# Kernel optimization log

Hardware: AMD Instinct MI355X
Metric: run time of the kernel (lower is better)

## Reference

```python
import jax, jax.numpy as jnp
import numpy as np

G, NPG = 100, 500
N = G * NPG            # 50000 nodes, contiguous equal-size graphs
IN, H = 128, 256
L = 3                  # num_layers
K = 3                  # knn k (loop=True -> self included)
E = 16 * N             # 800000 edges

def setup_inputs():
    key = jax.random.key(0)
    k = jax.random.split(key, 8)
    x = jax.random.normal(k[0], (N, IN), jnp.float32)
    batch = jnp.repeat(jnp.arange(G, dtype=jnp.int32), NPG)
    gid = jax.random.randint(k[1], (E,), 0, G)
    src = jax.random.randint(k[2], (E,), 0, NPG) + gid * NPG
    dst = jax.random.randint(k[3], (E,), 0, NPG) + gid * NPG
    edge_index = jnp.stack([src, dst]).astype(jnp.int32)
    def lin(kk, fin, fout):
        return (jax.random.normal(kk, (fin, fout), jnp.float32) / np.sqrt(fin)).astype(jnp.float32)
    inp = dict(x=x, edge_index=edge_index, batch=batch)
    inp["emb_W"] = lin(k[4], IN, H); inp["emb_b"] = jnp.zeros((H,), jnp.float32)
    inp["conv_W"] = jnp.stack([lin(jax.random.fold_in(k[5], i), H, H) for i in range(L)])
    inp["conv_b"] = jnp.zeros((L, H), jnp.float32)
    inp["fconv_W"] = jnp.stack([lin(jax.random.fold_in(k[6], i), H, H) for i in range(L)])
    inp["fconv_b"] = jnp.zeros((L, H), jnp.float32)
    inp["norm_w"] = jnp.ones((L, H), jnp.float32); inp["norm_b"] = jnp.zeros((L, H), jnp.float32); inp["norm_ms"] = jnp.ones((L, H), jnp.float32)
    inp["fnorm_w"] = jnp.ones((L, H), jnp.float32); inp["fnorm_b"] = jnp.zeros((L, H), jnp.float32); inp["fnorm_ms"] = jnp.ones((L, H), jnp.float32)
    inp["gate_W"] = lin(k[7], 2 * H, H); inp["gate_b"] = jnp.zeros((H,), jnp.float32)
    return inp

def _gcn_conv(h, src, dst, W, b):
    # GCNConv: add self loops, symmetric deg^-1/2 normalization
    m = h @ W                                     # [N,H]
    loop = jnp.arange(N, dtype=src.dtype)
    s2 = jnp.concatenate([src, loop]); d2 = jnp.concatenate([dst, loop])
    deg = jax.ops.segment_sum(jnp.ones_like(d2, jnp.float32), d2, num_segments=N)
    dinv = jnp.where(deg > 0, jax.lax.rsqrt(deg), 0.0)
    coef = (dinv[s2] * dinv[d2])[:, None]
    return jax.ops.segment_sum(m[s2] * coef, d2, num_segments=N) + b

def _graph_norm(x, batch, w, b, ms, cnt):
    # PyG GraphNorm: out = w * (x - ms*mean) / sqrt(var + eps) + b, per-graph stats
    mean = jax.ops.segment_sum(x, batch, num_segments=G) / cnt
    out = x - mean[batch] * ms
    var = jax.ops.segment_sum(out * out, batch, num_segments=G) / cnt
    return w * out * jax.lax.rsqrt(var + 1e-5)[batch] + b

def _knn_graph(x):
    # per-graph cosine knn, loop=True (self has sim 1 and is kept)
    xr = x.reshape(G, NPG, -1)
    xn = xr / (jnp.linalg.norm(xr, axis=-1, keepdims=True) + 1e-12)
    sim = jnp.einsum('gnh,gmh->gnm', xn, xn)      # [G,NPG,NPG]
    _, idx = jax.lax.top_k(sim, K)                # [G,NPG,K]
    offs = (jnp.arange(G) * NPG)[:, None, None]
    src = (idx + offs).reshape(-1)
    dst = jnp.broadcast_to(jnp.arange(N).reshape(G, NPG, 1), (G, NPG, K)).reshape(-1)
    return src.astype(jnp.int32), dst.astype(jnp.int32)

def reference(x, edge_index, batch, emb_W, emb_b, conv_W, conv_b, norm_w, norm_b, norm_ms, fconv_W, fconv_b, fnorm_w, fnorm_b, fnorm_ms, gate_W, gate_b):
    cnt = jax.ops.segment_sum(jnp.ones((N,), jnp.float32), batch, num_segments=G)[:, None]
    h = x @ emb_W + emb_b
    fsrc, fdst = _knn_graph(h)
    src, dst = edge_index[0], edge_index[1]
    all_x = []
    for i in range(L - 1):   # eval mode: dropout is identity
        prev = h
        h = _gcn_conv(h, src, dst, conv_W[i], conv_b[i])
        h = jax.nn.leaky_relu(_graph_norm(h, batch, norm_w[i], norm_b[i], norm_ms[i], cnt))
        f = _gcn_conv(h, fsrc, fdst, fconv_W[i], fconv_b[i])
        f = jax.nn.leaky_relu(_graph_norm(f, batch, fnorm_w[i], fnorm_b[i], fnorm_ms[i], cnt))
        gate = jax.nn.sigmoid(jnp.concatenate([h, f], axis=-1) @ gate_W + gate_b)
        h = gate * h + (1.0 - gate) * f + prev
        all_x.append(h)
    # faithful to source: for i in range(L): += pool(all_x[i-1])  (Python negative indexing!)
    gf = jnp.zeros((G, H), jnp.float32)
    for i in range(L):
        gf = gf + jax.ops.segment_sum(all_x[i - 1], batch, num_segments=G) / cnt
    return gf
```

## Files before the change

kernel.cpp:

```cpp
#include <hip/hip_runtime.h>
#include <math.h>

#define NN 50000
#define GG 100
#define NPGc 500
#define HH 256
#define IND 128

typedef __attribute__((ext_vector_type(8))) short short8v;
typedef __attribute__((ext_vector_type(4))) float f32x4;

__device__ __forceinline__ ushort f2bf(float f) {
    union { float f; unsigned u; } v; v.f = f;
    unsigned r = (v.u + 0x7fffu + ((v.u >> 16) & 1u)) >> 16;
    return (ushort)r;
}
__device__ __forceinline__ float bf2f(ushort h) {
    union { unsigned u; float f; } v; v.u = ((unsigned)h) << 16;
    return v.f;
}

__device__ __forceinline__ int swz(int row, int kidx) { return kidx ^ ((row & 7) << 3); }

__global__ void wcvt(const float* __restrict__ src, ushort* __restrict__ dst, int K, int N)
{
    int i = blockIdx.x * 256 + threadIdx.x;
    if (i < K * N) {
        int n = i / K, k = i % K;
        dst[i] = f2bf(src[(size_t)k * N + n]);
    }
}

__global__ __launch_bounds__(256)
void gemm_mfma(const void* __restrict__ Av, const void* __restrict__ A2v, int abf,
               const ushort* __restrict__ Wt, const float* __restrict__ bias,
               float* __restrict__ C, ushort* __restrict__ Cbf,
               int M, int K, int lda, int mode,
               const ushort* __restrict__ hn, const ushort* __restrict__ fn,
               const void* __restrict__ prevv, int prevbf)
{
    __shared__ ushort As[128][64];
    __shared__ ushort Bs[128][64];
    const int tid = threadIdx.x;
    const int lane = tid & 63;
    const int w = tid >> 6;
    const int wr = (w >> 1) * 64, wc = (w & 1) * 64;
    const int row0 = blockIdx.x * 128, col0 = blockIdx.y * 128;
    const int lr = lane & 15, lk = (lane >> 4) * 8;
    f32x4 acc[4][4] = {};

    for (int k0 = 0; k0 < K; k0 += 64) {
        __syncthreads();
        #pragma unroll
        for (int it = 0; it < 4; ++it) {
            int c = it * 256 + tid;
            int row = c >> 3, col = (c & 7) * 8;
            int gr = row0 + row; if (gr > M - 1) gr = M - 1;
            int kk = k0 + col;
            if (abf) {
                const ushort* Ap = (const ushort*)Av;
                if (A2v != nullptr && kk >= 256) { Ap = (const ushort*)A2v; kk -= 256; }
                *(int4*)&As[row][swz(row, col)] =
                    *(const int4*)&Ap[(size_t)gr * lda + kk];
            } else {
                const float* Ap = (const float*)Av;
                if (A2v != nullptr && kk >= 256) { Ap = (const float*)A2v; kk -= 256; }
                const float* s = &Ap[(size_t)gr * lda + kk];
                float4 v0 = *(const float4*)s;
                float4 v1 = *(const float4*)(s + 4);
                union { ushort u[8]; int4 q; } pk;
                pk.u[0] = f2bf(v0.x); pk.u[1] = f2bf(v0.y); pk.u[2] = f2bf(v0.z); pk.u[3] = f2bf(v0.w);
                pk.u[4] = f2bf(v1.x); pk.u[5] = f2bf(v1.y); pk.u[6] = f2bf(v1.z); pk.u[7] = f2bf(v1.w);
                *(int4*)&As[row][swz(row, col)] = pk.q;
            }
        }
        #pragma unroll
        for (int it = 0; it < 4; ++it) {
            int c = it * 256 + tid;
            int n = c >> 3, k = (c & 7) * 8;
            *(int4*)&Bs[n][swz(n, k)] = *(const int4*)&Wt[(size_t)(col0 + n) * K + k0 + k];
        }
        __syncthreads();
        #pragma unroll
        for (int ks = 0; ks < 2; ++ks) {
            short8v av[4], bv[4];
            #pragma unroll
            for (int m = 0; m < 4; ++m) {
                int rr = wr + m * 16 + lr;
                av[m] = *(const short8v*)&As[rr][swz(rr, ks * 32 + lk)];
            }
            #pragma unroll
            for (int n = 0; n < 4; ++n) {
                int rr = wc + n * 16 + lr;
                bv[n] = *(const short8v*)&Bs[rr][swz(rr, ks * 32 + lk)];
            }
            #pragma unroll
            for (int m = 0; m < 4; ++m)
                #pragma unroll
                for (int n = 0; n < 4; ++n)
                    acc[m][n] = __builtin_amdgcn_mfma_f32_16x16x32_bf16(av[m], bv[n], acc[m][n], 0, 0, 0);
        }
    }
    const int fr = (lane >> 4) * 4;
    if (mode == 0) {
        #pragma unroll
        for (int n = 0; n < 4; ++n) {
            int col = col0 + wc + n * 16 + lr;
            float bb = bias ? bias[col] : 0.f;
            #pragma unroll
            for (int m = 0; m < 4; ++m) {
                int rbase = row0 + wr + m * 16 + fr;
                #pragma unroll
                for (int r = 0; r < 4; ++r) {
                    int row = rbase + r;
                    if (row < M) C[(size_t)row * HH + col] = acc[m][n][r] + bb;
                }
            }
        }
    } else if (mode == 2) {
        #pragma unroll
        for (int n = 0; n < 4; ++n) {
            int col = col0 + wc + n * 16 + lr;
            float bb = bias ? bias[col] : 0.f;
            #pragma unroll
            for (int m = 0; m < 4; ++m) {
                int rbase = row0 + wr + m * 16 + fr;
                #pragma unroll
                for (int r = 0; r < 4; ++r) {
                    int row = rbase + r;
                    if (row < M) Cbf[(size_t)row * HH + col] = f2bf(acc[m][n][r] + bb);
                }
            }
        }
    } else {
        #pragma unroll
        for (int n = 0; n < 4; ++n) {
            int col = col0 + wc + n * 16 + lr;
            float gb = bias[col];
            #pragma unroll
            for (int m = 0; m < 4; ++m) {
                int rbase = row0 + wr + m * 16 + fr;
                #pragma unroll
                for (int r = 0; r < 4; ++r) {
                    int row = rbase + r;
                    if (row < M) {
                        size_t o = (size_t)row * HH + col;
                        float z = acc[m][n][r] + gb;
                        float s = 1.f / (1.f + expf(-z));
                        float hv = bf2f(hn[o]);
                        float fv = bf2f(fn[o]);
                        float pv = prevbf ? bf2f(((const ushort*)prevv)[o])
                                          : ((const float*)prevv)[o];
                        Cbf[o] = f2bf(s * hv + (1.f - s) * fv + pv);
                    }
                }
            }
        }
    }
}

__global__ __launch_bounds__(256)
void row_norm_hl(const float* __restrict__ h, ushort* __restrict__ xh, ushort* __restrict__ xl)
{
    int n = blockIdx.x, c = threadIdx.x;
    float v = h[(size_t)n * HH + c];
    __shared__ float red[256];
    red[c] = v * v;
    __syncthreads();
    for (int s = 128; s > 0; s >>= 1) {
        if (c < s) red[c] += red[c + s];
        __syncthreads();
    }
    float norm = sqrtf(red[0]);
    float xn = v / (norm + 1e-12f);
    ushort hi = f2bf(xn);
    xh[(size_t)n * HH + c] = hi;
    xl[(size_t)n * HH + c] = f2bf(xn - bf2f(hi));
}

__device__ __forceinline__ bool tk_better(float va, int ia, float vb, int ib)
{
    return (va > vb) || (va == vb && ia < ib);
}

__device__ __forceinline__ void ins3(float v, int i,
                                     float& a0, int& b0, float& a1, int& b1,
                                     float& a2, int& b2)
{
    if (tk_better(v, i, a0, b0))      { a2 = a1; b2 = b1; a1 = a0; b1 = b0; a0 = v; b0 = i; }
    else if (tk_better(v, i, a1, b1)) { a2 = a1; b2 = b1; a1 = v;  b1 = i; }
    else if (tk_better(v, i, a2, b2)) { a2 = v;  b2 = i; }
}

__device__ __forceinline__ void merge3(float& v0, float& v1, float& v2,
                                       int& i0, int& i1, int& i2, int off)
{
    float w0 = __shfl_xor(v0, off), w1 = __shfl_xor(v1, off), w2 = __shfl_xor(v2, off);
    int   j0 = __shfl_xor(i0, off), j1 = __shfl_xor(i1, off), j2 = __shfl_xor(i2, off);
    float avv[3] = { v0, v1, v2 }, bvv[3] = { w0, w1, w2 };
    int   aii[3] = { i0, i1, i2 }, bii[3] = { j0, j1, j2 };
    float rv[3]; int ri[3];
    int p = 0, q = 0;
    #pragma unroll
    for (int t = 0; t < 3; ++t) {
        bool takeA = tk_better(avv[p], aii[p], bvv[q], bii[q]);
        rv[t] = takeA ? avv[p] : bvv[q];
        ri[t] = takeA ? aii[p] : bii[q];
        if (takeA) ++p; else ++q;
    }
    v0 = rv[0]; v1 = rv[1]; v2 = rv[2];
    i0 = ri[0]; i1 = ri[1]; i2 = ri[2];
}

__global__ __launch_bounds__(256, 1)
void simtopk(const ushort* __restrict__ xnh, const ushort* __restrict__ xnl,
             int* __restrict__ fsrc)
{
    __shared__ ushort Bs[2][2][128][36];
    const int bid = blockIdx.x;
    const int xcd = bid & 7;
    const int rb  = (bid >> 3) & 7;
    const int g   = (bid >> 6) * 8 + xcd;
    if (g >= GG) return;
    const int row0 = rb * 64;
    const int tid  = threadIdx.x;
    const int lane = tid & 63;
    const int w    = tid >> 6;
    const int lr   = lane & 15;
    const int hi4  = lane >> 4;
    const size_t base = (size_t)g * NPGc * HH;

    int arow = row0 + w * 16 + lr; if (arow > NPGc - 1) arow = NPGc - 1;
    const ushort* aph = xnh + base + (size_t)arow * HH + hi4 * 8;
    const ushort* apl = xnl + base + (size_t)arow * HH + hi4 * 8;
    short8v ah[8], al[8];
    #pragma unroll
    for (int kc = 0; kc < 8; ++kc) {
        ah[kc] = *(const short8v*)(aph + kc * 32);
        al[kc] = *(const short8v*)(apl + kc * 32);
    }

    const int scol = tid >> 1;
    const int sq   = (tid & 1) * 2;

    float tv0[4], tv1[4], tv2[4];
    int   ti0[4], ti1[4], ti2[4];
    #pragma unroll
    for (int r = 0; r < 4; ++r) {
        tv0[r] = tv1[r] = tv2[r] = -2.f;
        ti0[r] = ti1[r] = ti2[r] = 0x7fffffff;
    }

    for (int ct = 0; ct < 4; ++ct) {
        const int col0 = ct * 128;
        int gcol = col0 + scol; if (gcol > NPGc - 1) gcol = NPGc - 1;
        const ushort* sph = xnh + base + (size_t)gcol * HH + sq * 8;
        const ushort* spl = xnl + base + (size_t)gcol * HH + sq * 8;

        {
            int4 h0 = *(const int4*)(sph);
            int4 h1 = *(const int4*)(sph + 8);
            int4 l0 = *(const int4*)(spl);
            int4 l1 = *(const int4*)(spl + 8);
            *(int4*)&Bs[0][0][scol][sq * 8]     = h0;
            *(int4*)&Bs[0][0][scol][sq * 8 + 8] = h1;
            *(int4*)&Bs[0][1][scol][sq * 8]     = l0;
            *(int4*)&Bs[0][1][scol][sq * 8 + 8] = l1;
        }
        __syncthreads();

        f32x4 acc[8] = {};
        #pragma unroll
        for (int kc = 0; kc < 8; ++kc) {
            const int cur = kc & 1, nxt = cur ^ 1;
            int4 h0, h1, l0, l1;
            if (kc < 7) {
                const ushort* nh = sph + (kc + 1) * 32;
                const ushort* nl = spl + (kc + 1) * 32;
                h0 = *(const int4*)(nh);
                h1 = *(const int4*)(nh + 8);
                l0 = *(const int4*)(nl);
                l1 = *(const int4*)(nl + 8);
            }
            short8v bh[8], bl[8];
            #pragma unroll
            for (int n = 0; n < 8; ++n) {
                int rr = n * 16 + lr;
                bh[n] = *(const short8v*)&Bs[cur][0][rr][hi4 * 8];
                bl[n] = *(const short8v*)&Bs[cur][1][rr][hi4 * 8];
            }
            #pragma unroll
            for (int n = 0; n < 8; ++n) {
                acc[n] = __builtin_amdgcn_mfma_f32_16x16x32_bf16(ah[kc], bh[n], acc[n], 0, 0, 0);
                acc[n] = __builtin_amdgcn_mfma_f32_16x16x32_bf16(ah[kc], bl[n], acc[n], 0, 0, 0);
                acc[n] = __builtin_amdgcn_mfma_f32_16x16x32_bf16(al[kc], bh[n], acc[n], 0, 0, 0);
            }
            if (kc < 7) {
                *(int4*)&Bs[nxt][0][scol][sq * 8]     = h0;
                *(int4*)&Bs[nxt][0][scol][sq * 8 + 8] = h1;
                *(int4*)&Bs[nxt][1][scol][sq * 8]     = l0;
                *(int4*)&Bs[nxt][1][scol][sq * 8 + 8] = l1;
            }
            __syncthreads();
        }

        #pragma unroll
        for (int r = 0; r < 4; ++r) {
            float a0 = tv0[r], a1 = tv1[r], a2 = tv2[r];
            int   b0 = ti0[r], b1 = ti1[r], b2 = ti2[r];
            #pragma unroll
            for (int n = 0; n < 8; ++n) {
                int col = col0 + n * 16 + lr;
                if (col < NPGc)
                    ins3(acc[n][r], col, a0, b0, a1, b1, a2, b2);
            }
            tv0[r] = a0; tv1[r] = a1; tv2[r] = a2;
            ti0[r] = b0; ti1[r] = b1; ti2[r] = b2;
        }
    }

    #pragma unroll
    for (int r = 0; r < 4; ++r) {
        float a0 = tv0[r], a1 = tv1[r], a2 = tv2[r];
        int   b0 = ti0[r], b1 = ti1[r], b2 = ti2[r];
        #pragma unroll
        for (int off = 1; off <= 8; off <<= 1)
            merge3(a0, a1, a2, b0, b1, b2, off);
        if (lr == 0) {
            int row = row0 + w * 16 + hi4 * 4 + r;
            if (row < NPGc) {
                int rg = g * NPGc + row;
                fsrc[rg * 3 + 0] = g * NPGc + b0;
                fsrc[rg * 3 + 1] = g * NPGc + b1;
                fsrc[rg * 3 + 2] = g * NPGc + b2;
            }
        }
    }
}

__global__ void hist_kernel(const int* __restrict__ dst, int* __restrict__ cnt, int nE)
{
    int e = blockIdx.x * 256 + threadIdx.x;
    if (e < nE) atomicAdd(&cnt[dst[e]], 1);
}

__global__ void scan1_kernel(const int* __restrict__ in, int* __restrict__ out,
                             int* __restrict__ bsum, int n)
{
    __shared__ int sh[256];
    int t = threadIdx.x;
    int i = blockIdx.x * 256 + t;
    int v = (i < n) ? in[i] : 0;
    sh[t] = v;
    __syncthreads();
    for (int s = 1; s < 256; s <<= 1) {
        int tv = (t >= s) ? sh[t - s] : 0;
        __syncthreads();
        sh[t] += tv;
        __syncthreads();
    }
    if (i < n) out[i] = sh[t] - v;
    if (t == 255) bsum[blockIdx.x] = sh[255];
}

__global__ void scan2_kernel(int* __restrict__ bsum, int nb)
{
    __shared__ int sh[256];
    int t = threadIdx.x;
    int v = (t < nb) ? bsum[t] : 0;
    sh[t] = v;
    __syncthreads();
    for (int s = 1; s < 256; s <<= 1) {
        int tv = (t >= s) ? sh[t - s] : 0;
        __syncthreads();
        sh[t] += tv;
        __syncthreads();
    }
    if (t < nb) bsum[t] = sh[t] - v;
}

__global__ void scan3_kernel(int* __restrict__ out, const int* __restrict__ bsum, int n)
{
    int i = blockIdx.x * 256 + threadIdx.x;
    if (i < n) out[i] += bsum[blockIdx.x];
}

__global__ void fill_kernel(const int* __restrict__ src, const int* __restrict__ dst,
                            const int* __restrict__ row_ptr, int* __restrict__ cursor,
                            int* __restrict__ sorted_src, int nE)
{
    int e = blockIdx.x * 256 + threadIdx.x;
    if (e < nE) {
        int d = dst[e];
        int pos = row_ptr[d] + atomicAdd(&cursor[d], 1);
        sorted_src[pos] = src[e];
    }
}

__global__ void dinv_kernel(const int* __restrict__ cnt, float* __restrict__ dinv, int n)
{
    int i = blockIdx.x * 256 + threadIdx.x;
    if (i < n) dinv[i] = rsqrtf((float)cnt[i] + 1.0f);
}

__global__ __launch_bounds__(256)
void gcn_gather(const ushort* __restrict__ m, const int* __restrict__ row_ptr,
                const int* __restrict__ cnt, const int* __restrict__ srcs,
                const float* __restrict__ dinv, const float* __restrict__ bias,
                ushort* __restrict__ out)
{
    int bid = blockIdx.x;
    int xcd = bid & 7, idx = bid >> 3;
    int g = xcd + 8 * (idx / NPGc);
    if (g >= GG) return;
    int n = g * NPGc + (idx % NPGc);
    int c = threadIdx.x;
    float dn = dinv[n];
    float acc = bf2f(m[(size_t)n * HH + c]) * dn;
    int s0 = row_ptr[n], e0 = s0 + cnt[n];
    for (int e = s0; e < e0; ++e) {
        int s = srcs[e];
        acc += bf2f(m[(size_t)s * HH + c]) * dinv[s];
    }
    out[(size_t)n * HH + c] = f2bf(acc * dn + bias[c]);
}

__global__ __launch_bounds__(256)
void fgcn_gather(const ushort* __restrict__ m, const int* __restrict__ fsrc,
                 const float* __restrict__ bias, ushort* __restrict__ out)
{
    int bid = blockIdx.x;
    int xcd = bid & 7, idx = bid >> 3;
    int g = xcd + 8 * (idx / NPGc);
    if (g >= GG) return;
    int n = g * NPGc + (idx % NPGc);
    int c = threadIdx.x;
    int s0 = fsrc[n * 3], s1 = fsrc[n * 3 + 1], s2 = fsrc[n * 3 + 2];
    float acc = bf2f(m[(size_t)n * HH + c]) + bf2f(m[(size_t)s0 * HH + c])
              + bf2f(m[(size_t)s1 * HH + c]) + bf2f(m[(size_t)s2 * HH + c]);
    out[(size_t)n * HH + c] = f2bf(0.25f * acc + bias[c]);
}

__global__ __launch_bounds__(256)
void norm_stats(const ushort* __restrict__ x, float* __restrict__ S1p, float* __restrict__ S2p)
{
    int g = blockIdx.x, chunk = blockIdx.y, c = threadIdx.x;
    int r0 = chunk * 63, r1 = min(r0 + 63, NPGc);
    float s1 = 0.f, s2 = 0.f;
    for (int r = r0; r < r1; ++r) {
        float v = bf2f(x[((size_t)(g * NPGc + r)) * HH + c]);
        s1 += v; s2 += v * v;
    }
    size_t o = ((size_t)(g * 8 + chunk)) * HH + c;
    S1p[o] = s1;
    S2p[o] = s2;
}

__global__ __launch_bounds__(256)
void norm_apply(ushort* __restrict__ x, const float* __restrict__ S1p, const float* __restrict__ S2p,
                const float* __restrict__ w, const float* __restrict__ b,
                const float* __restrict__ ms)
{
    int n = blockIdx.x, c = threadIdx.x;
    int g = n / NPGc;
    size_t o = (size_t)n * HH + c;
    float v = bf2f(x[o]);
    float s1 = 0.f, s2 = 0.f;
    #pragma unroll
    for (int j = 0; j < 8; ++j) {
        size_t po = ((size_t)(g * 8 + j)) * HH + c;
        s1 += S1p[po];
        s2 += S2p[po];
    }
    float mean = s1 / (float)NPGc;
    float mm = mean * ms[c];
    float var = s2 / (float)NPGc - 2.f * mm * mean + mm * mm;
    float outv = w[c] * (v - mm) * rsqrtf(var + 1e-5f) + b[c];
    x[o] = f2bf(outv > 0.f ? outv : 0.01f * outv);
}

__global__ __launch_bounds__(256)
void pool_kernel(const ushort* __restrict__ X0, const ushort* __restrict__ X1,
                 float* __restrict__ out)
{
    int g = blockIdx.x, c = threadIdx.x;
    float s0 = 0.f, s1 = 0.f;
    for (int r = 0; r < NPGc; ++r) {
        size_t o = ((size_t)(g * NPGc + r)) * HH + c;
        s0 += bf2f(X0[o]);
        s1 += bf2f(X1[o]);
    }
    out[g * HH + c] = (s0 + 2.f * s1) / (float)NPGc;
}

__global__ void sentinel_kernel(float* out, int n)
{
    int i = blockIdx.x * 256 + threadIdx.x;
    if (i < n) out[i] = 12345.0f;
}

extern "C" void kernel_launch(void* const* d_in, const int* in_sizes, int n_in,
                              void* d_out, int out_size, void* d_ws, size_t ws_size,
                              hipStream_t stream)
{
    const float* x       = (const float*)d_in[0];
    const int* edge_idx  = (const int*)d_in[1];
    const float* emb_W   = (const float*)d_in[3];
    const float* emb_b   = (const float*)d_in[4];
    const float* conv_W  = (const float*)d_in[5];
    const float* conv_b  = (const float*)d_in[6];
    const float* fconv_W = (const float*)d_in[7];
    const float* fconv_b = (const float*)d_in[8];
    const float* norm_w  = (const float*)d_in[9];
    const float* norm_b  = (const float*)d_in[10];
    const float* norm_ms = (const float*)d_in[11];
    const float* fnorm_w = (const float*)d_in[12];
    const float* fnorm_b = (const float*)d_in[13];
    const float* fnorm_ms= (const float*)d_in[14];
    const float* gate_W  = (const float*)d_in[15];
    const float* gate_b  = (const float*)d_in[16];

    const int E = in_sizes[1] / 2;
    const int* esrc = edge_idx;
    const int* edst = edge_idx + E;

    const size_t NHf = (size_t)NN * HH;
    char* p = (char*)d_ws;
    auto alloc = [&](size_t bytes) { char* r = p; p += (bytes + 255) & ~(size_t)255; return r; };
    float*  B0 = (float*)alloc(NHf * 4);
    ushort* Mr = (ushort*)alloc(NHf * 2);
    ushort* Ar = (ushort*)alloc(NHf * 2);
    ushort* Br = (ushort*)alloc(NHf * 2);
    ushort* H0 = (ushort*)alloc(NHf * 2);
    ushort* H1 = (ushort*)alloc(NHf * 2);
    ushort* xnh = Mr;
    ushort* xnl = Ar;
    int* sorted_src = (int*)alloc((size_t)E * 4);
    int* row_ptr    = (int*)alloc((size_t)NN * 4);
    int* deg_cnt    = (int*)alloc((size_t)NN * 4);
    int* cursor     = (int*)alloc((size_t)NN * 4);
    float* dinv     = (float*)alloc((size_t)NN * 4);
    int* fsrc       = (int*)alloc((size_t)NN * 3 * 4);
    float* S1p      = (float*)alloc((size_t)GG * 8 * HH * 4);
    float* S2p      = (float*)alloc((size_t)GG * 8 * HH * 4);
    int* bsum       = (int*)alloc(1024);
    ushort* wts     = (ushort*)alloc((size_t)425984 * 2);
    size_t needed = (size_t)(p - (char*)d_ws);
    if (ws_size < needed) {
        sentinel_kernel<<<(out_size + 255) / 256, 256, 0, stream>>>((float*)d_out, out_size);
        return;
    }
    ushort* embWt   = wts;
    ushort* convWt0 = wts + 32768;
    ushort* convWt1 = wts + 32768 + 65536;
    ushort* fconvWt0 = wts + 163840;
    ushort* fconvWt1 = wts + 163840 + 65536;
    ushort* gateWt  = wts + 294912;

    const int nScanB = (NN + 255) / 256;
    const int gatherGrid = 8 * 13 * NPGc;

    hipMemsetAsync(deg_cnt, 0, (size_t)NN * 4, stream);
    hipMemsetAsync(cursor, 0, (size_t)NN * 4, stream);

    wcvt<<<(32768 + 255) / 256, 256, 0, stream>>>(emb_W, embWt, IND, HH);
    wcvt<<<(65536 + 255) / 256, 256, 0, stream>>>(conv_W, convWt0, HH, HH);
    wcvt<<<(65536 + 255) / 256, 256, 0, stream>>>(conv_W + 65536, convWt1, HH, HH);
    wcvt<<<(65536 + 255) / 256, 256, 0, stream>>>(fconv_W, fconvWt0, HH, HH);
    wcvt<<<(65536 + 255) / 256, 256, 0, stream>>>(fconv_W + 65536, fconvWt1, HH, HH);
    wcvt<<<(131072 + 255) / 256, 256, 0, stream>>>(gate_W, gateWt, 2 * HH, HH);

    dim3 ggrid((NN + 127) / 128, 2);
    gemm_mfma<<<ggrid, 256, 0, stream>>>(x, nullptr, 0, embWt, emb_b, B0, nullptr,
                                         NN, IND, IND, 0, nullptr, nullptr, nullptr, 0);

    hist_kernel<<<(E + 255) / 256, 256, 0, stream>>>(edst, deg_cnt, E);
    scan1_kernel<<<nScanB, 256, 0, stream>>>(deg_cnt, row_ptr, bsum, NN);
    scan2_kernel<<<1, 256, 0, stream>>>(bsum, nScanB);
    scan3_kernel<<<nScanB, 256, 0, stream>>>(row_ptr, bsum, NN);
    fill_kernel<<<(E + 255) / 256, 256, 0, stream>>>(esrc, edst, row_ptr, cursor, sorted_src, E);
    dinv_kernel<<<(NN + 255) / 256, 256, 0, stream>>>(deg_cnt, dinv, NN);

    row_norm_hl<<<NN, 256, 0, stream>>>(B0, xnh, xnl);
    simtopk<<<832, 256, 0, stream>>>(xnh, xnl, fsrc);

    dim3 ngrid(GG, 8);
    const void* hptr = (const void*)B0;
    int habf = 0;
    ushort* Hout[2] = { H0, H1 };
    for (int i = 0; i < 2; ++i) {
        const ushort* Wc = (i == 0) ? convWt0 : convWt1;
        const ushort* Wf = (i == 0) ? fconvWt0 : fconvWt1;
        const float* bc  = conv_b  + (size_t)i * HH;
        const float* bf  = fconv_b + (size_t)i * HH;
        gemm_mfma<<<ggrid, 256, 0, stream>>>(hptr, nullptr, habf, Wc, nullptr, nullptr, Mr,
                                             NN, HH, HH, 2, nullptr, nullptr, nullptr, 0);
        gcn_gather<<<gatherGrid, 256, 0, stream>>>(Mr, row_ptr, deg_cnt, sorted_src,
                                                   dinv, bc, Ar);
        norm_stats<<<ngrid, 256, 0, stream>>>(Ar, S1p, S2p);
        norm_apply<<<NN, 256, 0, stream>>>(Ar, S1p, S2p, norm_w + i * HH, norm_b + i * HH,
                                           norm_ms + i * HH);
        gemm_mfma<<<ggrid, 256, 0, stream>>>(Ar, nullptr, 1, Wf, nullptr, nullptr, Mr,
                                             NN, HH, HH, 2, nullptr, nullptr, nullptr, 0);
        fgcn_gather<<<gatherGrid, 256, 0, stream>>>(Mr, fsrc, bf, Br);
        norm_stats<<<ngrid, 256, 0, stream>>>(Br, S1p, S2p);
        norm_apply<<<NN, 256, 0, stream>>>(Br, S1p, S2p, fnorm_w + i * HH, fnorm_b + i * HH,
                                           fnorm_ms + i * HH);
        gemm_mfma<<<ggrid, 256, 0, stream>>>(Ar, Br, 1, gateWt, gate_b, nullptr, Hout[i],
                                             NN, 2 * HH, HH, 1, Ar, Br, hptr, habf);
        hptr = (const void*)Hout[i];
        habf = 1;
    }
    pool_kernel<<<GG, 256, 0, stream>>>(H0, H1, (float*)d_out);
}
```

Baseline: 1.321 ms.

## Merge weight conversions, XCD-aware GEMM block mapping, precompute GraphNorm stats

Six weight-conversion launches are merged into one kernel. The GEMM switches to a 1D grid whose block index is remapped so that neighbouring row blocks and both column halves land on the same XCD, which should improve L2 reuse of the A tile. GraphNorm statistics are reduced once per graph into mean and rsqrt buffers by a new small kernel, so norm_apply no longer re-sums eight partials for every node. This adds two extra tiny launches per layer in exchange for fewer loads in norm_apply.

```diff
diff --git a/kernel.cpp b/kernel.cpp
--- a/kernel.cpp
+++ b/kernel.cpp
@@ -22,13 +22,20 @@
 
 __device__ __forceinline__ int swz(int row, int kidx) { return kidx ^ ((row & 7) << 3); }
 
-__global__ void wcvt(const float* __restrict__ src, ushort* __restrict__ dst, int K, int N)
+__global__ void wcvt_all(const float* __restrict__ emb_W, const float* __restrict__ conv_W,
+                         const float* __restrict__ fconv_W, const float* __restrict__ gate_W,
+                         ushort* __restrict__ dst)
 {
     int i = blockIdx.x * 256 + threadIdx.x;
-    if (i < K * N) {
-        int n = i / K, k = i % K;
-        dst[i] = f2bf(src[(size_t)k * N + n]);
-    }
+    if (i >= 425984) return;
+    float v;
+    if (i < 32768)       { int n = i >> 7, k = i & 127;              v = emb_W[(size_t)k * 256 + n]; }
+    else if (i < 98304)  { int j = i - 32768;  int n = j >> 8, k = j & 255; v = conv_W[(size_t)k * 256 + n]; }
+    else if (i < 163840) { int j = i - 98304;  int n = j >> 8, k = j & 255; v = conv_W[65536 + (size_t)k * 256 + n]; }
+    else if (i < 229376) { int j = i - 163840; int n = j >> 8, k = j & 255; v = fconv_W[(size_t)k * 256 + n]; }
+    else if (i < 294912) { int j = i - 229376; int n = j >> 8, k = j & 255; v = fconv_W[65536 + (size_t)k * 256 + n]; }
+    else                 { int j = i - 294912; int n = j >> 9, k = j & 511; v = gate_W[(size_t)k * 256 + n]; }
+    dst[i] = f2bf(v);
 }
 
 __global__ __launch_bounds__(256)
@@ -41,11 +48,18 @@
 {
     __shared__ ushort As[128][64];
     __shared__ ushort Bs[128][64];
+    const int bid = blockIdx.x;
+    const int xcd = bid & 7;
+    const int t = bid >> 3;
+    const int cb = t & 1;
+    const int rowblk = (t >> 1) * 8 + xcd;
+    const int row0 = rowblk * 128;
+    if (row0 >= M) return;
+    const int col0 = cb * 128;
     const int tid = threadIdx.x;
     const int lane = tid & 63;
     const int w = tid >> 6;
     const int wr = (w >> 1) * 64, wc = (w & 1) * 64;
-    const int row0 = blockIdx.x * 128, col0 = blockIdx.y * 128;
     const int lr = lane & 15, lk = (lane >> 4) * 8;
     f32x4 acc[4][4] = {};
 
@@ -457,14 +471,10 @@
 }
 
 __global__ __launch_bounds__(256)
-void norm_apply(ushort* __restrict__ x, const float* __restrict__ S1p, const float* __restrict__ S2p,
-                const float* __restrict__ w, const float* __restrict__ b,
-                const float* __restrict__ ms)
-{
-    int n = blockIdx.x, c = threadIdx.x;
-    int g = n / NPGc;
-    size_t o = (size_t)n * HH + c;
-    float v = bf2f(x[o]);
+void norm_reduce(const float* __restrict__ S1p, const float* __restrict__ S2p,
+                 const float* __restrict__ ms, float* __restrict__ MM, float* __restrict__ RS)
+{
+    int g = blockIdx.x, c = threadIdx.x;
     float s1 = 0.f, s2 = 0.f;
     #pragma unroll
     for (int j = 0; j < 8; ++j) {
@@ -475,7 +485,19 @@
     float mean = s1 / (float)NPGc;
     float mm = mean * ms[c];
     float var = s2 / (float)NPGc - 2.f * mm * mean + mm * mm;
-    float outv = w[c] * (v - mm) * rsqrtf(var + 1e-5f) + b[c];
+    MM[g * HH + c] = mm;
+    RS[g * HH + c] = rsqrtf(var + 1e-5f);
+}
+
+__global__ __launch_bounds__(256)
+void norm_apply(ushort* __restrict__ x, const float* __restrict__ MM, const float* __restrict__ RS,
+                const float* __restrict__ w, const float* __restrict__ b)
+{
+    int n = blockIdx.x, c = threadIdx.x;
+    int g = n / NPGc;
+    size_t o = (size_t)n * HH + c;
+    float v = bf2f(x[o]);
+    float outv = w[c] * (v - MM[g * HH + c]) * RS[g * HH + c] + b[c];
     x[o] = f2bf(outv > 0.f ? outv : 0.01f * outv);
 }
 
@@ -543,6 +565,8 @@
     int* fsrc       = (int*)alloc((size_t)NN * 3 * 4);
     float* S1p      = (float*)alloc((size_t)GG * 8 * HH * 4);
     float* S2p      = (float*)alloc((size_t)GG * 8 * HH * 4);
+    float* MM       = (float*)alloc((size_t)GG * HH * 4);
+    float* RS       = (float*)alloc((size_t)GG * HH * 4);
     int* bsum       = (int*)alloc(1024);
     ushort* wts     = (ushort*)alloc((size_t)425984 * 2);
     size_t needed = (size_t)(p - (char*)d_ws);
@@ -552,27 +576,22 @@
     }
     ushort* embWt   = wts;
     ushort* convWt0 = wts + 32768;
-    ushort* convWt1 = wts + 32768 + 65536;
+    ushort* convWt1 = wts + 98304;
     ushort* fconvWt0 = wts + 163840;
-    ushort* fconvWt1 = wts + 163840 + 65536;
+    ushort* fconvWt1 = wts + 229376;
     ushort* gateWt  = wts + 294912;
 
     const int nScanB = (NN + 255) / 256;
     const int gatherGrid = 8 * 13 * NPGc;
+    const int gemmGrid = 8 * 49 * 2;
 
     hipMemsetAsync(deg_cnt, 0, (size_t)NN * 4, stream);
     hipMemsetAsync(cursor, 0, (size_t)NN * 4, stream);
 
-    wcvt<<<(32768 + 255) / 256, 256, 0, stream>>>(emb_W, embWt, IND, HH);
-    wcvt<<<(65536 + 255) / 256, 256, 0, stream>>>(conv_W, convWt0, HH, HH);
-    wcvt<<<(65536 + 255) / 256, 256, 0, stream>>>(conv_W + 65536, convWt1, HH, HH);
-    wcvt<<<(65536 + 255) / 256, 256, 0, stream>>>(fconv_W, fconvWt0, HH, HH);
-    wcvt<<<(65536 + 255) / 256, 256, 0, stream>>>(fconv_W + 65536, fconvWt1, HH, HH);
-    wcvt<<<(131072 + 255) / 256, 256, 0, stream>>>(gate_W, gateWt, 2 * HH, HH);
-
-    dim3 ggrid((NN + 127) / 128, 2);
-    gemm_mfma<<<ggrid, 256, 0, stream>>>(x, nullptr, 0, embWt, emb_b, B0, nullptr,
-                                         NN, IND, IND, 0, nullptr, nullptr, nullptr, 0);
+    wcvt_all<<<1664, 256, 0, stream>>>(emb_W, conv_W, fconv_W, gate_W, wts);
+
+    gemm_mfma<<<gemmGrid, 256, 0, stream>>>(x, nullptr, 0, embWt, emb_b, B0, nullptr,
+                                            NN, IND, IND, 0, nullptr, nullptr, nullptr, 0);
 
     hist_kernel<<<(E + 255) / 256, 256, 0, stream>>>(edst, deg_cnt, E);
     scan1_kernel<<<nScanB, 256, 0, stream>>>(deg_cnt, row_ptr, bsum, NN);
@@ -593,21 +612,21 @@
         const ushort* Wf = (i == 0) ? fconvWt0 : fconvWt1;
         const float* bc  = conv_b  + (size_t)i * HH;
         const float* bf  = fconv_b + (size_t)i * HH;
-        gemm_mfma<<<ggrid, 256, 0, stream>>>(hptr, nullptr, habf, Wc, nullptr, nullptr, Mr,
-                                             NN, HH, HH, 2, nullptr, nullptr, nullptr, 0);
+        gemm_mfma<<<gemmGrid, 256, 0, stream>>>(hptr, nullptr, habf, Wc, nullptr, nullptr, Mr,
+                                                NN, HH, HH, 2, nullptr, nullptr, nullptr, 0);
         gcn_gather<<<gatherGrid, 256, 0, stream>>>(Mr, row_ptr, deg_cnt, sorted_src,
                                                    dinv, bc, Ar);
         norm_stats<<<ngrid, 256, 0, stream>>>(Ar, S1p, S2p);
-        norm_apply<<<NN, 256, 0, stream>>>(Ar, S1p, S2p, norm_w + i * HH, norm_b + i * HH,
-                                           norm_ms + i * HH);
-        gemm_mfma<<<ggrid, 256, 0, stream>>>(Ar, nullptr, 1, Wf, nullptr, nullptr, Mr,
-                                             NN, HH, HH, 2, nullptr, nullptr, nullptr, 0);
+        norm_reduce<<<GG, 256, 0, stream>>>(S1p, S2p, norm_ms + i * HH, MM, RS);
+        norm_apply<<<NN, 256, 0, stream>>>(Ar, MM, RS, norm_w + i * HH, norm_b + i * HH);
+        gemm_mfma<<<gemmGrid, 256, 0, stream>>>(Ar, nullptr, 1, Wf, nullptr, nullptr, Mr,
+                                                NN, HH, HH, 2, nullptr, nullptr, nullptr, 0);
         fgcn_gather<<<gatherGrid, 256, 0, stream>>>(Mr, fsrc, bf, Br);
         norm_stats<<<ngrid, 256, 0, stream>>>(Br, S1p, S2p);
-        norm_apply<<<NN, 256, 0, stream>>>(Br, S1p, S2p, fnorm_w + i * HH, fnorm_b + i * HH,
-                                           fnorm_ms + i * HH);
-        gemm_mfma<<<ggrid, 256, 0, stream>>>(Ar, Br, 1, gateWt, gate_b, nullptr, Hout[i],
-                                             NN, 2 * HH, HH, 1, Ar, Br, hptr, habf);
+        norm_reduce<<<GG, 256, 0, stream>>>(S1p, S2p, fnorm_ms + i * HH, MM, RS);
+        norm_apply<<<NN, 256, 0, stream>>>(Br, MM, RS, fnorm_w + i * HH, fnorm_b + i * HH);
+        gemm_mfma<<<gemmGrid, 256, 0, stream>>>(Ar, Br, 1, gateWt, gate_b, nullptr, Hout[i],
+                                                NN, 2 * HH, HH, 1, Ar, Br, hptr, habf);
         hptr = (const void*)Hout[i];
         habf = 1;
     }
```

New measurement: 1.264 ms. 4.3% less time.
